# Kernel optimization log

Hardware: AMD Instinct MI355X
Metric: run time of the kernel (lower is better)

## Reference

```python
import jax, jax.numpy as jnp
import numpy as np


def _conv1x1(x, w, b):
    # x: [B, Cin, H, W], w: [Cout, Cin], b: [Cout]
    return jnp.einsum('oi,bihw->bohw', w, x) + b[None, :, None, None]


def setup_inputs() -> dict:
    key = jax.random.key(0)
    ks = jax.random.split(key, 16)
    B, H, W = 32, 512, 512
    img = jax.random.normal(ks[0], (B, 3, H, W), dtype=jnp.float32)
    mask = jax.random.uniform(ks[1], (B, 1, H, W), dtype=jnp.float32)

    def init_conv(k, cout, cin):
        k1, k2 = jax.random.split(k)
        bound = 1.0 / np.sqrt(cin)  # PyTorch Conv2d default init range
        w = jax.random.uniform(k1, (cout, cin), minval=-bound, maxval=bound, dtype=jnp.float32)
        b = jax.random.uniform(k2, (cout,), minval=-bound, maxval=bound, dtype=jnp.float32)
        return w, b

    qi_w, qi_b = init_conv(ks[2], 1, 3)
    ki_w, ki_b = init_conv(ks[3], 1, 3)
    vi_w, vi_b = init_conv(ks[4], 3, 3)
    qr_w, qr_b = init_conv(ks[5], 1, 1)
    kr_w, kr_b = init_conv(ks[6], 1, 1)
    vr_w, vr_b = init_conv(ks[7], 1, 1)
    fu_w, fu_b = init_conv(ks[8], 3, 6)
    return {
        'img': img, 'mask': mask,
        'qi_w': qi_w, 'qi_b': qi_b, 'ki_w': ki_w, 'ki_b': ki_b,
        'vi_w': vi_w, 'vi_b': vi_b, 'qr_w': qr_w, 'qr_b': qr_b,
        'kr_w': kr_w, 'kr_b': kr_b, 'vr_w': vr_w, 'vr_b': vr_b,
        'fu_w': fu_w, 'fu_b': fu_b,
    }


def reference(img, mask, qi_w, qi_b, ki_w, ki_b, vi_w, vi_b,
              qr_w, qr_b, kr_w, kr_b, vr_w, vr_b, fu_w, fu_b):
    q_i = _conv1x1(img, qi_w, qi_b)    # [B,1,H,W]
    k_i = _conv1x1(img, ki_w, ki_b)    # [B,1,H,W]
    v_i = _conv1x1(img, vi_w, vi_b)    # [B,3,H,W]
    q_r = _conv1x1(mask, qr_w, qr_b)   # [B,1,H,W]
    k_r = _conv1x1(mask, kr_w, kr_b)   # [B,1,H,W]
    v_r = _conv1x1(mask, vr_w, vr_b)   # [B,1,H,W]
    # broadcasting: the v_r terms are 1-channel and broadcast to 3 channels
    f_i = jax.nn.sigmoid(q_i * k_i) * v_i + jax.nn.sigmoid(q_i * k_r) * v_r  # [B,3,H,W]
    f_r = jax.nn.sigmoid(q_r * k_r) * v_r + jax.nn.sigmoid(q_r * k_i) * v_i  # [B,3,H,W]
    f_f = _conv1x1(jnp.concatenate([f_i, f_r], axis=1), fu_w, fu_b)          # [B,3,H,W]
    return f_f
```

## Files before the change

### kernel.cpp

```cpp
#include <hip/hip_runtime.h>
#include <math.h>


#define HW_SHIFT 18
#define HWQ_SHIFT 16

__device__ __forceinline__ float sigm(float x) {
    return __builtin_amdgcn_rcpf(1.0f + __expf(-x));
}

__global__ __launch_bounds__(256) void rim_kernel(
    const float* __restrict__ img,  const float* __restrict__ mask,
    const float* __restrict__ qiw,  const float* __restrict__ qib,
    const float* __restrict__ kiw,  const float* __restrict__ kib,
    const float* __restrict__ viw,  const float* __restrict__ vib,
    const float* __restrict__ qrw,  const float* __restrict__ qrb,
    const float* __restrict__ krw,  const float* __restrict__ krb,
    const float* __restrict__ vrw,  const float* __restrict__ vrb,
    const float* __restrict__ fuw,  const float* __restrict__ fub,
    float* __restrict__ out)
{
    const int HWQ = 1 << HWQ_SHIFT;
    const int n4  = 32 * HWQ;

    const float w_qi0 = qiw[0], w_qi1 = qiw[1], w_qi2 = qiw[2], b_qi = qib[0];
    const float w_ki0 = kiw[0], w_ki1 = kiw[1], w_ki2 = kiw[2], b_ki = kib[0];
    float w_vi[9], b_vi[3];
#pragma unroll
    for (int j = 0; j < 9; ++j) w_vi[j] = viw[j];
#pragma unroll
    for (int j = 0; j < 3; ++j) b_vi[j] = vib[j];
    const float w_qr = qrw[0], b_qr = qrb[0];
    const float w_kr = krw[0], b_kr = krb[0];
    const float w_vr = vrw[0], b_vr = vrb[0];
    float w_fu[18], b_fu[3];
#pragma unroll
    for (int j = 0; j < 18; ++j) w_fu[j] = fuw[j];
#pragma unroll
    for (int j = 0; j < 3; ++j) b_fu[j] = fub[j];

    const int tid    = blockIdx.x * blockDim.x + threadIdx.x;
    const int stride = gridDim.x * blockDim.x;

    for (int i = tid; i < n4; i += stride) {
        const int b   = i >> HWQ_SHIFT;
        const int hw4 = i & (HWQ - 1);

        const float4* ip = (const float4*)(img  + ((size_t)b * 3 << HW_SHIFT)) + hw4;
        const float4* mp = (const float4*)(mask + ((size_t)b     << HW_SHIFT)) + hw4;
        float4 x0 = ip[0];
        float4 x1 = ip[HWQ];
        float4 x2 = ip[2 * HWQ];
        float4 mm = mp[0];

        float4 o0, o1, o2;
        float* px0 = &x0.x; float* px1 = &x1.x; float* px2 = &x2.x;
        float* pm  = &mm.x;
        float* po0 = &o0.x; float* po1 = &o1.x; float* po2 = &o2.x;

#pragma unroll
        for (int l = 0; l < 4; ++l) {
            const float X0 = px0[l], X1 = px1[l], X2 = px2[l], M = pm[l];

            const float q_i = b_qi + w_qi0 * X0 + w_qi1 * X1 + w_qi2 * X2;
            const float k_i = b_ki + w_ki0 * X0 + w_ki1 * X1 + w_ki2 * X2;
            const float v0  = b_vi[0] + w_vi[0] * X0 + w_vi[1] * X1 + w_vi[2] * X2;
            const float v1  = b_vi[1] + w_vi[3] * X0 + w_vi[4] * X1 + w_vi[5] * X2;
            const float v2  = b_vi[2] + w_vi[6] * X0 + w_vi[7] * X1 + w_vi[8] * X2;
            const float q_r = b_qr + w_qr * M;
            const float k_r = b_kr + w_kr * M;
            const float v_r = b_vr + w_vr * M;

            const float s_ii = sigm(q_i * k_i);
            const float s_ir = sigm(q_i * k_r);
            const float s_rr = sigm(q_r * k_r);
            const float s_ri = sigm(q_r * k_i);

            const float fi0 = s_ii * v0 + s_ir * v_r;
            const float fi1 = s_ii * v1 + s_ir * v_r;
            const float fi2 = s_ii * v2 + s_ir * v_r;
            const float fr0 = s_rr * v_r + s_ri * v0;
            const float fr1 = s_rr * v_r + s_ri * v1;
            const float fr2 = s_rr * v_r + s_ri * v2;

            po0[l] = b_fu[0] + w_fu[0]  * fi0 + w_fu[1]  * fi1 + w_fu[2]  * fi2
                             + w_fu[3]  * fr0 + w_fu[4]  * fr1 + w_fu[5]  * fr2;
            po1[l] = b_fu[1] + w_fu[6]  * fi0 + w_fu[7]  * fi1 + w_fu[8]  * fi2
                             + w_fu[9]  * fr0 + w_fu[10] * fr1 + w_fu[11] * fr2;
            po2[l] = b_fu[2] + w_fu[12] * fi0 + w_fu[13] * fi1 + w_fu[14] * fi2
                             + w_fu[15] * fr0 + w_fu[16] * fr1 + w_fu[17] * fr2;
        }

        float4* op = (float4*)(out + ((size_t)b * 3 << HW_SHIFT)) + hw4;
        op[0]       = o0;
        op[HWQ]     = o1;
        op[2 * HWQ] = o2;
    }
}

extern "C" void kernel_launch(void* const* d_in, const int* in_sizes, int n_in,
                              void* d_out, int out_size, void* d_ws, size_t ws_size,
                              hipStream_t stream) {
    const float* img  = (const float*)d_in[0];
    const float* mask = (const float*)d_in[1];
    const float* qiw  = (const float*)d_in[2];
    const float* qib  = (const float*)d_in[3];
    const float* kiw  = (const float*)d_in[4];
    const float* kib  = (const float*)d_in[5];
    const float* viw  = (const float*)d_in[6];
    const float* vib  = (const float*)d_in[7];
    const float* qrw  = (const float*)d_in[8];
    const float* qrb  = (const float*)d_in[9];
    const float* krw  = (const float*)d_in[10];
    const float* krb  = (const float*)d_in[11];
    const float* vrw  = (const float*)d_in[12];
    const float* vrb  = (const float*)d_in[13];
    const float* fuw  = (const float*)d_in[14];
    const float* fub  = (const float*)d_in[15];
    float* out = (float*)d_out;

    rim_kernel<<<2048, 256, 0, stream>>>(img, mask, qiw, qib, kiw, kib, viw, vib,
                                         qrw, qrb, krw, krb, vrw, vrb, fuw, fub, out);
}
```

Measured before the change: 235.4 us.

## Batch four float4 loads per thread up front and use nontemporal stores

Replaces the grid-stride loop with a fixed mapping where each thread handles four float4 groups, 256 apart. All 16 vector loads are issued before any compute, with a sched_barrier keeping them grouped. This raises memory-level parallelism and hides load latency in a streaming kernel. Outputs use nontemporal stores to avoid polluting the cache, and launch bounds request 4 blocks per CU. The cost is higher register pressure from holding 16 vectors, and the mapping now depends on the grid exactly covering the input.

```diff
diff --git a/kernel.cpp b/kernel.cpp
--- a/kernel.cpp
+++ b/kernel.cpp
@@ -2,14 +2,17 @@
 #include <math.h>
 
 
-#define HW_SHIFT 18
+#define HW_SHIFT  18
 #define HWQ_SHIFT 16
+#define HWQ (1 << HWQ_SHIFT)
+
+typedef float vf4 __attribute__((ext_vector_type(4)));
 
 __device__ __forceinline__ float sigm(float x) {
     return __builtin_amdgcn_rcpf(1.0f + __expf(-x));
 }
 
-__global__ __launch_bounds__(256) void rim_kernel(
+__global__ __launch_bounds__(256, 4) void rim_kernel(
     const float* __restrict__ img,  const float* __restrict__ mask,
     const float* __restrict__ qiw,  const float* __restrict__ qib,
     const float* __restrict__ kiw,  const float* __restrict__ kib,
@@ -20,9 +23,6 @@
     const float* __restrict__ fuw,  const float* __restrict__ fub,
     float* __restrict__ out)
 {
-    const int HWQ = 1 << HWQ_SHIFT;
-    const int n4  = 32 * HWQ;
-
     const float w_qi0 = qiw[0], w_qi1 = qiw[1], w_qi2 = qiw[2], b_qi = qib[0];
     const float w_ki0 = kiw[0], w_ki1 = kiw[1], w_ki2 = kiw[2], b_ki = kib[0];
     float w_vi[9], b_vi[3];
@@ -39,28 +39,32 @@
 #pragma unroll
     for (int j = 0; j < 3; ++j) b_fu[j] = fub[j];
 
-    const int tid    = blockIdx.x * blockDim.x + threadIdx.x;
-    const int stride = gridDim.x * blockDim.x;
+    const int g0 = blockIdx.x * 1024 + threadIdx.x;
+    const int b  = g0 >> HWQ_SHIFT;
+    const int hw = g0 & (HWQ - 1);
 
-    for (int i = tid; i < n4; i += stride) {
-        const int b   = i >> HWQ_SHIFT;
-        const int hw4 = i & (HWQ - 1);
+    const vf4* ip = (const vf4*)(img  + ((size_t)b * 3 << HW_SHIFT));
+    const vf4* mp = (const vf4*)(mask + ((size_t)b     << HW_SHIFT));
 
-        const float4* ip = (const float4*)(img  + ((size_t)b * 3 << HW_SHIFT)) + hw4;
-        const float4* mp = (const float4*)(mask + ((size_t)b     << HW_SHIFT)) + hw4;
-        float4 x0 = ip[0];
-        float4 x1 = ip[HWQ];
-        float4 x2 = ip[2 * HWQ];
-        float4 mm = mp[0];
+    vf4 x0[4], x1[4], x2[4], mq[4];
+#pragma unroll
+    for (int k = 0; k < 4; ++k) {
+        const int h = hw + k * 256;
+        x0[k] = ip[h];
+        x1[k] = ip[h + HWQ];
+        x2[k] = ip[h + 2 * HWQ];
+        mq[k] = mp[h];
+    }
+    __builtin_amdgcn_sched_barrier(0);
 
-        float4 o0, o1, o2;
-        float* px0 = &x0.x; float* px1 = &x1.x; float* px2 = &x2.x;
-        float* pm  = &mm.x;
-        float* po0 = &o0.x; float* po1 = &o1.x; float* po2 = &o2.x;
+    float* op = out + ((size_t)b * 3 << HW_SHIFT);
 
 #pragma unroll
+    for (int k = 0; k < 4; ++k) {
+        vf4 o0, o1, o2;
+#pragma unroll
         for (int l = 0; l < 4; ++l) {
-            const float X0 = px0[l], X1 = px1[l], X2 = px2[l], M = pm[l];
+            const float X0 = x0[k][l], X1 = x1[k][l], X2 = x2[k][l], M = mq[k][l];
 
             const float q_i = b_qi + w_qi0 * X0 + w_qi1 * X1 + w_qi2 * X2;
             const float k_i = b_ki + w_ki0 * X0 + w_ki1 * X1 + w_ki2 * X2;
@@ -83,18 +87,17 @@
             const float fr1 = s_rr * v_r + s_ri * v1;
             const float fr2 = s_rr * v_r + s_ri * v2;
 
-            po0[l] = b_fu[0] + w_fu[0]  * fi0 + w_fu[1]  * fi1 + w_fu[2]  * fi2
-                             + w_fu[3]  * fr0 + w_fu[4]  * fr1 + w_fu[5]  * fr2;
-            po1[l] = b_fu[1] + w_fu[6]  * fi0 + w_fu[7]  * fi1 + w_fu[8]  * fi2
-                             + w_fu[9]  * fr0 + w_fu[10] * fr1 + w_fu[11] * fr2;
-            po2[l] = b_fu[2] + w_fu[12] * fi0 + w_fu[13] * fi1 + w_fu[14] * fi2
-                             + w_fu[15] * fr0 + w_fu[16] * fr1 + w_fu[17] * fr2;
+            o0[l] = b_fu[0] + w_fu[0]  * fi0 + w_fu[1]  * fi1 + w_fu[2]  * fi2
+                            + w_fu[3]  * fr0 + w_fu[4]  * fr1 + w_fu[5]  * fr2;
+            o1[l] = b_fu[1] + w_fu[6]  * fi0 + w_fu[7]  * fi1 + w_fu[8]  * fi2
+                            + w_fu[9]  * fr0 + w_fu[10] * fr1 + w_fu[11] * fr2;
+            o2[l] = b_fu[2] + w_fu[12] * fi0 + w_fu[13] * fi1 + w_fu[14] * fi2
+                            + w_fu[15] * fr0 + w_fu[16] * fr1 + w_fu[17] * fr2;
         }
-
-        float4* op = (float4*)(out + ((size_t)b * 3 << HW_SHIFT)) + hw4;
-        op[0]       = o0;
-        op[HWQ]     = o1;
-        op[2 * HWQ] = o2;
+        const int h = hw + k * 256;
+        __builtin_nontemporal_store(o0, (vf4*)(op + 4 * (size_t)h));
+        __builtin_nontemporal_store(o1, (vf4*)(op + 4 * ((size_t)h + HWQ)));
+        __builtin_nontemporal_store(o2, (vf4*)(op + 4 * ((size_t)h + 2 * HWQ)));
     }
 }
 
```

Result: no change. 234.9 us (-0.2%).
